# Kernel optimization log

Hardware: AMD Instinct MI355X
Metric: run time of the kernel (lower is better)

Reference implementation:

```python
import jax, jax.numpy as jnp
import numpy as np

N_USER = 50000
N_ITEM = 50000
D_IN = 128
D_OUT = 128
N_EDGE = 600000


def _sage(x_src, x_dst, ei, Wl, bl, Wr):
    # PyG SAGEConv: out = lin_l(mean_{j in N(i)} x_j) + lin_r(x_i)
    # lin_l has bias, lin_r has no bias. Weights are [out, in].
    src, dst = ei[0], ei[1]
    n_dst = x_dst.shape[0]
    msg = x_src[src]                                            # [E, D_in] gather
    agg = jax.ops.segment_sum(msg, dst, num_segments=n_dst)     # [N_dst, D_in]
    cnt = jax.ops.segment_sum(jnp.ones((ei.shape[1],), x_src.dtype), dst,
                              num_segments=n_dst)
    mean = agg / jnp.maximum(cnt, 1.0)[:, None]                 # isolated nodes -> 0
    return mean @ Wl.T + bl + x_dst @ Wr.T


def setup_inputs() -> dict:
    key = jax.random.key(0)
    ks = jax.random.split(key, 16)
    inp = {
        "x_user": jax.random.normal(ks[0], (N_USER, D_IN), jnp.float32),
        "x_item": jax.random.normal(ks[1], (N_ITEM, D_IN), jnp.float32),
        "ei_rates": jax.random.randint(ks[2], (2, N_EDGE), 0, N_USER, jnp.int64 if jax.config.jax_enable_x64 else jnp.int32),
        "ei_rev": jax.random.randint(ks[3], (2, N_EDGE), 0, N_USER, jnp.int64 if jax.config.jax_enable_x64 else jnp.int32),
        "ei_follows": jax.random.randint(ks[4], (2, N_EDGE), 0, N_USER, jnp.int64 if jax.config.jax_enable_x64 else jnp.int32),
    }
    s = 1.0 / np.sqrt(D_IN)
    names = ["rates", "rev", "fol"]
    for i, nm in enumerate(names):
        inp[f"Wl_{nm}"] = jax.random.uniform(ks[5 + 3 * i], (D_OUT, D_IN), jnp.float32, -s, s)
        inp[f"bl_{nm}"] = jax.random.uniform(ks[6 + 3 * i], (D_OUT,), jnp.float32, -s, s)
        inp[f"Wr_{nm}"] = jax.random.uniform(ks[7 + 3 * i], (D_OUT, D_IN), jnp.float32, -s, s)
    return inp


def reference(x_user, x_item, ei_rates, ei_rev, ei_follows,
              Wl_rates, bl_rates, Wr_rates,
              Wl_rev, bl_rev, Wr_rev,
              Wl_fol, bl_fol, Wr_fol):
    # relation (user -rates-> item): src=user, dst=item
    out_item = _sage(x_user, x_item, ei_rates, Wl_rates, bl_rates, Wr_rates)
    # relation (item -rev_rates-> user): src=item, dst=user
    out_user_rev = _sage(x_item, x_user, ei_rev, Wl_rev, bl_rev, Wr_rev)
    # relation (user -follows-> user)
    out_user_fol = _sage(x_user, x_user, ei_follows, Wl_fol, bl_fol, Wr_fol)
    # HeteroConv aggr='mean': average relation outputs per dst node type
    out_user = (out_user_rev + out_user_fol) * 0.5
    return out_user, out_item
```

## Files before the change

kernel.cpp:

```cpp
#include <hip/hip_runtime.h>

#define D 128
#define NBB 392

typedef __attribute__((ext_vector_type(8))) short bf16x8;
typedef __attribute__((ext_vector_type(4))) float f32x4;

__device__ inline unsigned short f2bf(float f) {
  unsigned u = __builtin_bit_cast(unsigned, f);
  unsigned r = u + 0x7FFFu + ((u >> 16) & 1u);
  return (unsigned short)(r >> 16);
}
__device__ inline float bf2f(unsigned short b) {
  unsigned u = ((unsigned)b) << 16;
  return __builtin_bit_cast(float, u);
}

__global__ void __launch_bounds__(256) conv2_kernel(
    const float* __restrict__ xu, const float* __restrict__ xi,
    unsigned short* __restrict__ xbu, unsigned short* __restrict__ xbi,
    int n4u, int n4i) {
  int i = blockIdx.x * 256 + threadIdx.x;
  const float* x;
  unsigned short* xb;
  if (i < n4u) { x = xu; xb = xbu; }
  else { i -= n4u; if (i >= n4i) return; x = xi; xb = xbi; }
  float4 v = ((const float4*)x)[i];
  ushort4 o;
  o.x = f2bf(v.x); o.y = f2bf(v.y); o.z = f2bf(v.z); o.w = f2bf(v.w);
  ((ushort4*)xb)[i] = o;
}

struct Rel3 { const int* ei[3]; int ne[3]; int nb[3]; };

__global__ void __launch_bounds__(256) bhist_kernel(Rel3 R, int* __restrict__ bh) {
  int b = blockIdx.x, rel = 0;
  while (b >= R.nb[rel]) { b -= R.nb[rel]; rel++; }
  __shared__ int lh[NBB];
  for (int t = threadIdx.x; t < NBB; t += 256) lh[t] = 0;
  __syncthreads();
  const int ne = R.ne[rel];
  const int* dsts = R.ei[rel] + ne;
  const int base = b * 2048;
#pragma unroll
  for (int k = 0; k < 8; k++) {
    int i = base + k * 256 + threadIdx.x;
    if (i < ne) atomicAdd(&lh[dsts[i] >> 7], 1);
  }
  __syncthreads();
  for (int t = threadIdx.x; t < NBB; t += 256)
    if (lh[t]) atomicAdd(&bh[rel * NBB + t], lh[t]);
}

__global__ void __launch_bounds__(192) scanb_kernel(const int* __restrict__ bh,
                                                    int* __restrict__ bbase,
                                                    int* __restrict__ bcur, int nbkt) {
  int w = threadIdx.x >> 6, l = threadIdx.x & 63;
  if (w >= 3) return;
  const int off = w * NBB;
  int v[7];
  int s0 = 0;
#pragma unroll
  for (int k = 0; k < 7; k++) {
    int idx = l * 7 + k;
    v[k] = (idx < nbkt) ? bh[off + idx] : 0;
    s0 += v[k];
  }
  int s = s0;
  for (int dlt = 1; dlt < 64; dlt <<= 1) {
    int t = __shfl_up(s, dlt);
    if (l >= dlt) s += t;
  }
  int run = s - s0;
#pragma unroll
  for (int k = 0; k < 7; k++) {
    int idx = l * 7 + k;
    if (idx < nbkt) { bbase[off + idx] = run; bcur[off + idx] = run; run += v[k]; }
  }
  if (l == 63) bbase[off + nbkt] = run;
}

struct PArgs { const int* ei[3]; int ne[3]; int nb[3]; unsigned* part[3]; };

__global__ void __launch_bounds__(256) part_kernel(PArgs P, int* __restrict__ bcur,
                                                   int nbkt) {
  int b = blockIdx.x, rel = 0;
  while (b >= P.nb[rel]) { b -= P.nb[rel]; rel++; }
  const int ne = P.ne[rel];
  const int* src = P.ei[rel];
  const int* dst = src + ne;
  const int base = b * 4096;
  const int tn = min(4096, ne - base);
  __shared__ int lh[NBB], lscan[NBB], gb[NBB], lcur[NBB];
  __shared__ uint2 pairs[4096];
  const int tid = threadIdx.x;
  for (int t = tid; t < NBB; t += 256) lh[t] = 0;
  __syncthreads();
#pragma unroll
  for (int k = 0; k < 16; k++) {
    int i = base + k * 256 + tid;
    if (i < ne) atomicAdd(&lh[dst[i] >> 7], 1);
  }
  __syncthreads();
  if (tid < 64) {
    int v[7];
    int s0 = 0;
#pragma unroll
    for (int k = 0; k < 7; k++) {
      int idx = tid * 7 + k;
      v[k] = (idx < NBB) ? lh[idx] : 0;
      s0 += v[k];
    }
    int s = s0;
    for (int dlt = 1; dlt < 64; dlt <<= 1) {
      int t = __shfl_up(s, dlt);
      if (tid >= dlt) s += t;
    }
    int run = s - s0;
#pragma unroll
    for (int k = 0; k < 7; k++) {
      int idx = tid * 7 + k;
      if (idx < NBB) { lscan[idx] = run; run += v[k]; }
    }
  }
  __syncthreads();
  for (int t = tid; t < nbkt; t += 256) {
    gb[t] = atomicAdd(&bcur[rel * NBB + t], lh[t]);
    lcur[t] = lscan[t];
  }
  __syncthreads();
#pragma unroll
  for (int k = 0; k < 16; k++) {
    int i = base + k * 256 + tid;
    if (i < ne) {
      int d = dst[i];
      int slot = atomicAdd(&lcur[d >> 7], 1);
      pairs[slot] = (uint2){(unsigned)src[i], (unsigned)d};
    }
  }
  __syncthreads();
  unsigned* __restrict__ out = P.part[rel];
#pragma unroll
  for (int k = 0; k < 16; k++) {
    int slot = k * 256 + tid;
    if (slot < tn) {
      uint2 p = pairs[slot];
      int bin = (int)(p.y >> 7);
      out[gb[bin] + (slot - lscan[bin])] = p.x | ((p.y & 127u) << 25);
    }
  }
}

struct S2Args {
  const unsigned* part[3];
  int* rp[3];
  int* es[3];
  int m[3];
};

__global__ void __launch_bounds__(256) sort2_kernel(S2Args A, const int* __restrict__ bbase,
                                                    int nbkt) {
  const int rel = blockIdx.x / nbkt;
  const int b = blockIdx.x - rel * nbkt;
  const int bs = bbase[rel * NBB + b];
  const int be = bbase[rel * NBB + b + 1];
  const int n = be - bs;
  const unsigned* __restrict__ pp = A.part[rel] + bs;
  int* __restrict__ es = A.es[rel];
  const int tid = threadIdx.x;
  __shared__ unsigned stage[4096];
  __shared__ int lcnt[128], lofs[128], lcur[128];
  if (tid < 128) lcnt[tid] = 0;
  __syncthreads();
  const bool staged = (n <= 4096);
  if (staged) {
    for (int i = tid; i < n; i += 256) {
      unsigned p = pp[i];
      stage[i] = p;
      atomicAdd(&lcnt[p >> 25], 1);
    }
  } else {
    for (int i = tid; i < n; i += 256) atomicAdd(&lcnt[pp[i] >> 25], 1);
  }
  __syncthreads();
  if (tid < 64) {
    int v0 = lcnt[2 * tid], v1 = lcnt[2 * tid + 1];
    int s0 = v0 + v1;
    int s = s0;
    for (int dlt = 1; dlt < 64; dlt <<= 1) {
      int t = __shfl_up(s, dlt);
      if (tid >= dlt) s += t;
    }
    int ex = s - s0;
    lofs[2 * tid] = ex;
    lofs[2 * tid + 1] = ex + v0;
  }
  __syncthreads();
  if (tid < 128) {
    int gdst = b * 128 + tid;
    if (gdst < A.m[rel]) A.rp[rel][gdst] = bs + lofs[tid];
    lcur[tid] = lofs[tid];
  }
  if (b == nbkt - 1 && tid == 0) A.rp[rel][A.m[rel]] = bbase[rel * NBB + nbkt];
  __syncthreads();
  if (staged) {
    for (int i = tid; i < n; i += 256) {
      unsigned p = stage[i];
      int slot = atomicAdd(&lcur[p >> 25], 1);
      es[bs + slot] = (int)(p & 0x1FFFFFFu);
    }
  } else {
    for (int i = tid; i < n; i += 256) {
      unsigned p = pp[i];
      int slot = atomicAdd(&lcur[p >> 25], 1);
      es[bs + slot] = (int)(p & 0x1FFFFFFu);
    }
  }
}

struct GatherArgs {
  const unsigned short* xb[3];
  const int* rp[3];
  const int* es[3];
  unsigned short* mean[3];
  int m[3];
  int nb[3];
};

__global__ void __launch_bounds__(256) gather3_kernel(GatherArgs G) {
  int b = blockIdx.x, rel = 0;
  while (b >= G.nb[rel]) { b -= G.nb[rel]; rel++; }
  int row = b * 4 + (threadIdx.x >> 6);
  if (row >= G.m[rel]) return;
  const int lane = threadIdx.x & 63;
  const unsigned short* __restrict__ xb = G.xb[rel];
  const int* __restrict__ rowptr = G.rp[rel];
  const int* __restrict__ esrc = G.es[rel];
  const int beg = rowptr[row], end = rowptr[row + 1];
  const size_t loff = lane * 2;
  float a0 = 0.f, a1 = 0.f, b0 = 0.f, b1 = 0.f;
  float c0 = 0.f, c1 = 0.f, d0 = 0.f, d1 = 0.f;
  int j = beg;
  for (; j + 4 <= end; j += 4) {
    int s0 = esrc[j], s1 = esrc[j + 1], s2 = esrc[j + 2], s3 = esrc[j + 3];
    unsigned v0 = *(const unsigned*)(xb + (size_t)s0 * D + loff);
    unsigned v1 = *(const unsigned*)(xb + (size_t)s1 * D + loff);
    unsigned v2 = *(const unsigned*)(xb + (size_t)s2 * D + loff);
    unsigned v3 = *(const unsigned*)(xb + (size_t)s3 * D + loff);
    a0 += bf2f((unsigned short)(v0 & 0xFFFFu)); a1 += bf2f((unsigned short)(v0 >> 16));
    b0 += bf2f((unsigned short)(v1 & 0xFFFFu)); b1 += bf2f((unsigned short)(v1 >> 16));
    c0 += bf2f((unsigned short)(v2 & 0xFFFFu)); c1 += bf2f((unsigned short)(v2 >> 16));
    d0 += bf2f((unsigned short)(v3 & 0xFFFFu)); d1 += bf2f((unsigned short)(v3 >> 16));
  }
  for (; j < end; j++) {
    int s = esrc[j];
    unsigned v = *(const unsigned*)(xb + (size_t)s * D + loff);
    a0 += bf2f((unsigned short)(v & 0xFFFFu)); a1 += bf2f((unsigned short)(v >> 16));
  }
  a0 += (b0 + c0) + d0;
  a1 += (b1 + c1) + d1;
  float inv = 1.0f / (float)max(end - beg, 1);
  unsigned o = (unsigned)f2bf(a0 * inv) | ((unsigned)f2bf(a1 * inv) << 16);
  *(unsigned*)(G.mean[rel] + (size_t)row * D + loff) = o;
}

__global__ void __launch_bounds__(384) prep_kernel(
    const float* __restrict__ Wl_rates, const float* __restrict__ Wr_rates, const float* __restrict__ bl_rates,
    const float* __restrict__ Wl_rev, const float* __restrict__ Wr_rev, const float* __restrict__ bl_rev,
    const float* __restrict__ Wl_fol, const float* __restrict__ Wr_fol, const float* __restrict__ bl_fol,
    unsigned short* __restrict__ Wb_user, unsigned short* __restrict__ Wb_item,
    float* __restrict__ b_user, float* __restrict__ b_item) {
  int n = blockIdx.x;
  int k = threadIdx.x;
  float v;
  if (k < 128)      v = 0.5f * Wl_rev[n * 128 + k];
  else if (k < 256) v = 0.5f * Wl_fol[n * 128 + (k - 128)];
  else              v = 0.5f * (Wr_rev[n * 128 + (k - 256)] + Wr_fol[n * 128 + (k - 256)]);
  Wb_user[n * 384 + k] = f2bf(v);
  if (k < 256) {
    float w = (k < 128) ? Wl_rates[n * 128 + k] : Wr_rates[n * 128 + (k - 128)];
    Wb_item[n * 256 + k] = f2bf(w);
  }
  if (n == 0 && k < 128) {
    b_item[k] = bl_rates[k];
    b_user[k] = 0.5f * (bl_rev[k] + bl_fol[k]);
  }
}

struct BSrcs { const unsigned short* s[3]; };
struct GemmArgs {
  BSrcs su, si;
  const unsigned short* wbU; const unsigned short* wbI;
  const float* bU; const float* bI;
  float* outU; float* outI;
  int MU, MI, nbU;
};

__global__ void __launch_bounds__(256) gemm2_kernel(GemmArgs A) {
  const bool isU = (int)blockIdx.x < A.nbU;
  const int bid = isU ? blockIdx.x : blockIdx.x - A.nbU;
  const BSrcs S = isU ? A.su : A.si;
  const unsigned short* __restrict__ Wb = isU ? A.wbU : A.wbI;
  const int K = isU ? 384 : 256;
  const float* __restrict__ bias = isU ? A.bU : A.bI;
  float* __restrict__ out = isU ? A.outU : A.outI;
  const int M = isU ? A.MU : A.MI;

  __shared__ __align__(16) unsigned short As[64][72];
  __shared__ __align__(16) unsigned short Ws[128][72];
  const int tid = threadIdx.x;
  const int lane = tid & 63;
  const int wave = tid >> 6;
  const int wrow = (wave >> 1) * 32;
  const int wcol = (wave & 1) * 64;
  const int l15 = lane & 15;
  const int quad = lane >> 4;
  const int m0 = bid * 64;

  f32x4 acc[2][4];
#pragma unroll
  for (int r = 0; r < 2; r++)
#pragma unroll
    for (int c = 0; c < 4; c++) acc[r][c] = (f32x4){0.f, 0.f, 0.f, 0.f};

  const int nchunks = K >> 6;
  for (int ch = 0; ch < nchunks; ch++) {
    const unsigned short* sp = S.s[ch >> 1];
    const int coff = (ch & 1) << 6;
    {
      int row = tid >> 2, part = tid & 3;
      int m = m0 + row;
      uint4 v0 = {0, 0, 0, 0}, v1 = {0, 0, 0, 0};
      if (m < M) {
        const uint4* g = (const uint4*)(sp + (size_t)m * D + coff + part * 16);
        v0 = g[0]; v1 = g[1];
      }
      uint4* ld = (uint4*)(&As[row][part * 16]);
      ld[0] = v0; ld[1] = v1;
    }
    {
      int n = tid >> 1, half = tid & 1;
      const uint4* g = (const uint4*)(Wb + (size_t)n * K + ch * 64 + half * 32);
      uint4* ld = (uint4*)(&Ws[n][half * 32]);
      ld[0] = g[0]; ld[1] = g[1]; ld[2] = g[2]; ld[3] = g[3];
    }
    __syncthreads();
#pragma unroll
    for (int kk = 0; kk < 64; kk += 32) {
      const int kb = kk + quad * 8;
      bf16x8 a0 = *(const bf16x8*)&As[wrow + l15][kb];
      bf16x8 a1 = *(const bf16x8*)&As[wrow + 16 + l15][kb];
      bf16x8 b0 = *(const bf16x8*)&Ws[wcol + l15][kb];
      bf16x8 b1 = *(const bf16x8*)&Ws[wcol + 16 + l15][kb];
      bf16x8 b2 = *(const bf16x8*)&Ws[wcol + 32 + l15][kb];
      bf16x8 b3 = *(const bf16x8*)&Ws[wcol + 48 + l15][kb];
      acc[0][0] = __builtin_amdgcn_mfma_f32_16x16x32_bf16(a0, b0, acc[0][0], 0, 0, 0);
      acc[0][1] = __builtin_amdgcn_mfma_f32_16x16x32_bf16(a0, b1, acc[0][1], 0, 0, 0);
      acc[0][2] = __builtin_amdgcn_mfma_f32_16x16x32_bf16(a0, b2, acc[0][2], 0, 0, 0);
      acc[0][3] = __builtin_amdgcn_mfma_f32_16x16x32_bf16(a0, b3, acc[0][3], 0, 0, 0);
      acc[1][0] = __builtin_amdgcn_mfma_f32_16x16x32_bf16(a1, b0, acc[1][0], 0, 0, 0);
      acc[1][1] = __builtin_amdgcn_mfma_f32_16x16x32_bf16(a1, b1, acc[1][1], 0, 0, 0);
      acc[1][2] = __builtin_amdgcn_mfma_f32_16x16x32_bf16(a1, b2, acc[1][2], 0, 0, 0);
      acc[1][3] = __builtin_amdgcn_mfma_f32_16x16x32_bf16(a1, b3, acc[1][3], 0, 0, 0);
    }
    __syncthreads();
  }
#pragma unroll
  for (int c = 0; c < 4; c++) {
    const int n = wcol + c * 16 + l15;
    const float bv = bias[n];
#pragma unroll
    for (int r = 0; r < 2; r++) {
      const int mrow = m0 + wrow + r * 16 + quad * 4;
#pragma unroll
      for (int i = 0; i < 4; i++) {
        if (mrow + i < M) out[(size_t)(mrow + i) * D + n] = acc[r][c][i] + bv;
      }
    }
  }
}

extern "C" void kernel_launch(void* const* d_in, const int* in_sizes, int n_in,
                              void* d_out, int out_size, void* d_ws, size_t ws_size,
                              hipStream_t stream) {
  const float* x_user   = (const float*)d_in[0];
  const float* x_item   = (const float*)d_in[1];
  const int*   ei_rates = (const int*)d_in[2];
  const int*   ei_rev   = (const int*)d_in[3];
  const int*   ei_fol   = (const int*)d_in[4];
  const float* Wl_rates = (const float*)d_in[5];
  const float* bl_rates = (const float*)d_in[6];
  const float* Wr_rates = (const float*)d_in[7];
  const float* Wl_rev   = (const float*)d_in[8];
  const float* bl_rev   = (const float*)d_in[9];
  const float* Wr_rev   = (const float*)d_in[10];
  const float* Wl_fol   = (const float*)d_in[11];
  const float* bl_fol   = (const float*)d_in[12];
  const float* Wr_fol   = (const float*)d_in[13];

  const int NU = in_sizes[0] / D;
  const int NI = in_sizes[1] / D;
  const int E_rates = in_sizes[2] / 2;
  const int E_rev   = in_sizes[3] / 2;
  const int E_fol   = in_sizes[4] / 2;
  const int nbkt = ((NU > NI ? NU : NI) + 127) / 128;

  char* wsb = (char*)d_ws;
  size_t off = 0;
  auto take = [&](size_t bytes) {
    char* p = wsb + off;
    off += (bytes + 15) & ~(size_t)15;
    return p;
  };
  int* bhist = (int*)take(3 * NBB * 4);
  const size_t zero_bytes = off;
  int* bbase = (int*)take(3 * NBB * 4);
  int* bcur  = (int*)take(3 * NBB * 4);
  unsigned* part_rates = (unsigned*)take((size_t)E_rates * 4);
  unsigned* part_rev   = (unsigned*)take((size_t)E_rev * 4);
  unsigned* part_fol   = (unsigned*)take((size_t)E_fol * 4);
  int* es_rates = (int*)take((size_t)E_rates * 4);
  int* es_rev   = (int*)take((size_t)E_rev * 4);
  int* es_fol   = (int*)take((size_t)E_fol * 4);
  int* rp_rates = (int*)take((size_t)(NI + 1) * 4);
  int* rp_rev   = (int*)take((size_t)(NU + 1) * 4);
  int* rp_fol   = (int*)take((size_t)(NU + 1) * 4);
  unsigned short* xb_user    = (unsigned short*)take((size_t)NU * D * 2);
  unsigned short* xb_item    = (unsigned short*)take((size_t)NI * D * 2);
  unsigned short* mean_rates = (unsigned short*)take((size_t)NI * D * 2);
  unsigned short* mean_rev   = (unsigned short*)take((size_t)NU * D * 2);
  unsigned short* mean_fol   = (unsigned short*)take((size_t)NU * D * 2);
  unsigned short* Wb_user    = (unsigned short*)take(128 * 384 * 2);
  unsigned short* Wb_item    = (unsigned short*)take(128 * 256 * 2);
  float* b_user = (float*)take(128 * 4);
  float* b_item = (float*)take(128 * 4);

  hipMemsetAsync(d_ws, 0, zero_bytes, stream);
  prep_kernel<<<128, 384, 0, stream>>>(Wl_rates, Wr_rates, bl_rates,
                                       Wl_rev, Wr_rev, bl_rev,
                                       Wl_fol, Wr_fol, bl_fol,
                                       Wb_user, Wb_item, b_user, b_item);
  {
    int n4u = NU * D / 4, n4i = NI * D / 4;
    conv2_kernel<<<(n4u + n4i + 255) / 256, 256, 0, stream>>>(
        x_user, x_item, xb_user, xb_item, n4u, n4i);
  }

  Rel3 R;
  R.ei[0] = ei_rates; R.ne[0] = E_rates; R.nb[0] = (E_rates + 2047) / 2048;
  R.ei[1] = ei_rev;   R.ne[1] = E_rev;   R.nb[1] = (E_rev + 2047) / 2048;
  R.ei[2] = ei_fol;   R.ne[2] = E_fol;   R.nb[2] = (E_fol + 2047) / 2048;
  bhist_kernel<<<R.nb[0] + R.nb[1] + R.nb[2], 256, 0, stream>>>(R, bhist);

  scanb_kernel<<<1, 192, 0, stream>>>(bhist, bbase, bcur, nbkt);

  PArgs P;
  P.ei[0] = ei_rates; P.ne[0] = E_rates; P.nb[0] = (E_rates + 4095) / 4096; P.part[0] = part_rates;
  P.ei[1] = ei_rev;   P.ne[1] = E_rev;   P.nb[1] = (E_rev + 4095) / 4096;   P.part[1] = part_rev;
  P.ei[2] = ei_fol;   P.ne[2] = E_fol;   P.nb[2] = (E_fol + 4095) / 4096;   P.part[2] = part_fol;
  part_kernel<<<P.nb[0] + P.nb[1] + P.nb[2], 256, 0, stream>>>(P, bcur, nbkt);

  S2Args S2;
  S2.part[0] = part_rates; S2.rp[0] = rp_rates; S2.es[0] = es_rates; S2.m[0] = NI;
  S2.part[1] = part_rev;   S2.rp[1] = rp_rev;   S2.es[1] = es_rev;   S2.m[1] = NU;
  S2.part[2] = part_fol;   S2.rp[2] = rp_fol;   S2.es[2] = es_fol;   S2.m[2] = NU;
  sort2_kernel<<<3 * nbkt, 256, 0, stream>>>(S2, bbase, nbkt);

  GatherArgs ga;
  ga.xb[0] = xb_user; ga.rp[0] = rp_rates; ga.es[0] = es_rates; ga.mean[0] = mean_rates;
  ga.m[0] = NI; ga.nb[0] = (NI + 3) / 4;
  ga.xb[1] = xb_item; ga.rp[1] = rp_rev;   ga.es[1] = es_rev;   ga.mean[1] = mean_rev;
  ga.m[1] = NU; ga.nb[1] = (NU + 3) / 4;
  ga.xb[2] = xb_user; ga.rp[2] = rp_fol;   ga.es[2] = es_fol;   ga.mean[2] = mean_fol;
  ga.m[2] = NU; ga.nb[2] = (NU + 3) / 4;
  gather3_kernel<<<ga.nb[0] + ga.nb[1] + ga.nb[2], 256, 0, stream>>>(ga);

  GemmArgs gma;
  gma.su.s[0] = mean_rev;   gma.su.s[1] = mean_fol; gma.su.s[2] = xb_user;
  gma.si.s[0] = mean_rates; gma.si.s[1] = xb_item;  gma.si.s[2] = nullptr;
  gma.wbU = Wb_user; gma.wbI = Wb_item;
  gma.bU = b_user;   gma.bI = b_item;
  gma.outU = (float*)d_out;
  gma.outI = (float*)d_out + (size_t)NU * D;
  gma.MU = NU; gma.MI = NI;
  gma.nbU = (NU + 63) / 64;
  const int nbI = (NI + 63) / 64;
  gemm2_kernel<<<gma.nbU + nbI, 256, 0, stream>>>(gma);
}
```

Measured before the change: 313.7 us.

## Fuse bucket sort with neighbor gather and enlarge GEMM row tile

Merges the per-bucket counting sort and the mean-aggregation gather into one kernel. Each block sorts its 128-destination bucket into shared memory and immediately aggregates neighbor features, so the es/rowptr arrays are never written to or read back from global memory and one launch disappears. Each block now handles 128 rows with only 4 waves, which may lower parallelism in the gather phase. Oversized buckets fall back to a slow per-row linear scan. The GEMM tile also doubles to 128 rows per block with 4x4 MFMA accumulators per wave, clamping row loads instead of zero-filling them.

```diff
diff --git a/kernel.cpp b/kernel.cpp
--- a/kernel.cpp
+++ b/kernel.cpp
@@ -151,117 +151,104 @@
   }
 }
 
-struct S2Args {
+struct BAArgs {
   const unsigned* part[3];
-  int* rp[3];
-  int* es[3];
+  const unsigned short* xb[3];
+  unsigned short* mean[3];
   int m[3];
 };
 
-__global__ void __launch_bounds__(256) sort2_kernel(S2Args A, const int* __restrict__ bbase,
-                                                    int nbkt) {
+__global__ void __launch_bounds__(256) bagg_kernel(BAArgs A, const int* __restrict__ bbase,
+                                                   int nbkt) {
   const int rel = blockIdx.x / nbkt;
   const int b = blockIdx.x - rel * nbkt;
   const int bs = bbase[rel * NBB + b];
   const int be = bbase[rel * NBB + b + 1];
   const int n = be - bs;
   const unsigned* __restrict__ pp = A.part[rel] + bs;
-  int* __restrict__ es = A.es[rel];
+  const unsigned short* __restrict__ x = A.xb[rel];
+  unsigned short* __restrict__ mean = A.mean[rel];
+  const int m = A.m[rel];
   const int tid = threadIdx.x;
-  __shared__ unsigned stage[4096];
+  const int w = tid >> 6, lane = tid & 63;
+  const size_t loff = lane * 2;
+  __shared__ unsigned sorted[4096];
   __shared__ int lcnt[128], lofs[128], lcur[128];
-  if (tid < 128) lcnt[tid] = 0;
-  __syncthreads();
-  const bool staged = (n <= 4096);
-  if (staged) {
-    for (int i = tid; i < n; i += 256) {
-      unsigned p = pp[i];
-      stage[i] = p;
-      atomicAdd(&lcnt[p >> 25], 1);
-    }
-  } else {
+
+  if (n <= 4096) {
+    if (tid < 128) lcnt[tid] = 0;
+    __syncthreads();
     for (int i = tid; i < n; i += 256) atomicAdd(&lcnt[pp[i] >> 25], 1);
-  }
-  __syncthreads();
-  if (tid < 64) {
-    int v0 = lcnt[2 * tid], v1 = lcnt[2 * tid + 1];
-    int s0 = v0 + v1;
-    int s = s0;
-    for (int dlt = 1; dlt < 64; dlt <<= 1) {
-      int t = __shfl_up(s, dlt);
-      if (tid >= dlt) s += t;
-    }
-    int ex = s - s0;
-    lofs[2 * tid] = ex;
-    lofs[2 * tid + 1] = ex + v0;
-  }
-  __syncthreads();
-  if (tid < 128) {
-    int gdst = b * 128 + tid;
-    if (gdst < A.m[rel]) A.rp[rel][gdst] = bs + lofs[tid];
-    lcur[tid] = lofs[tid];
-  }
-  if (b == nbkt - 1 && tid == 0) A.rp[rel][A.m[rel]] = bbase[rel * NBB + nbkt];
-  __syncthreads();
-  if (staged) {
-    for (int i = tid; i < n; i += 256) {
-      unsigned p = stage[i];
-      int slot = atomicAdd(&lcur[p >> 25], 1);
-      es[bs + slot] = (int)(p & 0x1FFFFFFu);
-    }
-  } else {
+    __syncthreads();
+    if (tid < 64) {
+      int v0 = lcnt[2 * tid], v1 = lcnt[2 * tid + 1];
+      int s0 = v0 + v1, s = s0;
+      for (int dlt = 1; dlt < 64; dlt <<= 1) {
+        int t = __shfl_up(s, dlt);
+        if (tid >= dlt) s += t;
+      }
+      int ex = s - s0;
+      lofs[2 * tid] = ex;
+      lofs[2 * tid + 1] = ex + v0;
+    }
+    __syncthreads();
+    if (tid < 128) lcur[tid] = lofs[tid];
+    __syncthreads();
     for (int i = tid; i < n; i += 256) {
       unsigned p = pp[i];
       int slot = atomicAdd(&lcur[p >> 25], 1);
-      es[bs + slot] = (int)(p & 0x1FFFFFFu);
-    }
-  }
-}
-
-struct GatherArgs {
-  const unsigned short* xb[3];
-  const int* rp[3];
-  const int* es[3];
-  unsigned short* mean[3];
-  int m[3];
-  int nb[3];
-};
-
-__global__ void __launch_bounds__(256) gather3_kernel(GatherArgs G) {
-  int b = blockIdx.x, rel = 0;
-  while (b >= G.nb[rel]) { b -= G.nb[rel]; rel++; }
-  int row = b * 4 + (threadIdx.x >> 6);
-  if (row >= G.m[rel]) return;
-  const int lane = threadIdx.x & 63;
-  const unsigned short* __restrict__ xb = G.xb[rel];
-  const int* __restrict__ rowptr = G.rp[rel];
-  const int* __restrict__ esrc = G.es[rel];
-  const int beg = rowptr[row], end = rowptr[row + 1];
-  const size_t loff = lane * 2;
-  float a0 = 0.f, a1 = 0.f, b0 = 0.f, b1 = 0.f;
-  float c0 = 0.f, c1 = 0.f, d0 = 0.f, d1 = 0.f;
-  int j = beg;
-  for (; j + 4 <= end; j += 4) {
-    int s0 = esrc[j], s1 = esrc[j + 1], s2 = esrc[j + 2], s3 = esrc[j + 3];
-    unsigned v0 = *(const unsigned*)(xb + (size_t)s0 * D + loff);
-    unsigned v1 = *(const unsigned*)(xb + (size_t)s1 * D + loff);
-    unsigned v2 = *(const unsigned*)(xb + (size_t)s2 * D + loff);
-    unsigned v3 = *(const unsigned*)(xb + (size_t)s3 * D + loff);
-    a0 += bf2f((unsigned short)(v0 & 0xFFFFu)); a1 += bf2f((unsigned short)(v0 >> 16));
-    b0 += bf2f((unsigned short)(v1 & 0xFFFFu)); b1 += bf2f((unsigned short)(v1 >> 16));
-    c0 += bf2f((unsigned short)(v2 & 0xFFFFu)); c1 += bf2f((unsigned short)(v2 >> 16));
-    d0 += bf2f((unsigned short)(v3 & 0xFFFFu)); d1 += bf2f((unsigned short)(v3 >> 16));
-  }
-  for (; j < end; j++) {
-    int s = esrc[j];
-    unsigned v = *(const unsigned*)(xb + (size_t)s * D + loff);
-    a0 += bf2f((unsigned short)(v & 0xFFFFu)); a1 += bf2f((unsigned short)(v >> 16));
-  }
-  a0 += (b0 + c0) + d0;
-  a1 += (b1 + c1) + d1;
-  float inv = 1.0f / (float)max(end - beg, 1);
-  unsigned o = (unsigned)f2bf(a0 * inv) | ((unsigned)f2bf(a1 * inv) << 16);
-  *(unsigned*)(G.mean[rel] + (size_t)row * D + loff) = o;
+      sorted[slot] = p & 0x1FFFFFFu;
+    }
+    __syncthreads();
+    for (int r = w; r < 128; r += 4) {
+      int gdst = b * 128 + r;
+      if (gdst >= m) break;
+      const int beg = lofs[r], end = lcur[r];
+      float a0 = 0.f, a1 = 0.f, b0 = 0.f, b1 = 0.f;
+      float c0 = 0.f, c1 = 0.f, d0 = 0.f, d1 = 0.f;
+      int j = beg;
+      for (; j + 4 <= end; j += 4) {
+        unsigned s0 = sorted[j], s1 = sorted[j + 1], s2 = sorted[j + 2], s3 = sorted[j + 3];
+        unsigned v0 = *(const unsigned*)(x + (size_t)s0 * D + loff);
+        unsigned v1 = *(const unsigned*)(x + (size_t)s1 * D + loff);
+        unsigned v2 = *(const unsigned*)(x + (size_t)s2 * D + loff);
+        unsigned v3 = *(const unsigned*)(x + (size_t)s3 * D + loff);
+        a0 += bf2f((unsigned short)(v0 & 0xFFFFu)); a1 += bf2f((unsigned short)(v0 >> 16));
+        b0 += bf2f((unsigned short)(v1 & 0xFFFFu)); b1 += bf2f((unsigned short)(v1 >> 16));
+        c0 += bf2f((unsigned short)(v2 & 0xFFFFu)); c1 += bf2f((unsigned short)(v2 >> 16));
+        d0 += bf2f((unsigned short)(v3 & 0xFFFFu)); d1 += bf2f((unsigned short)(v3 >> 16));
+      }
+      for (; j < end; j++) {
+        unsigned s = sorted[j];
+        unsigned v = *(const unsigned*)(x + (size_t)s * D + loff);
+        a0 += bf2f((unsigned short)(v & 0xFFFFu)); a1 += bf2f((unsigned short)(v >> 16));
+      }
+      a0 += (b0 + c0) + d0;
+      a1 += (b1 + c1) + d1;
+      float inv = 1.0f / (float)max(end - beg, 1);
+      unsigned o = (unsigned)f2bf(a0 * inv) | ((unsigned)f2bf(a1 * inv) << 16);
+      *(unsigned*)(mean + (size_t)gdst * D + loff) = o;
+    }
+  } else {
+    for (int r = w; r < 128; r += 4) {
+      int gdst = b * 128 + r;
+      if (gdst >= m) break;
+      float a0 = 0.f, a1 = 0.f;
+      int cnt = 0;
+      for (int j = 0; j < n; j++) {
+        unsigned p = pp[j];
+        if ((int)(p >> 25) == r) {
+          unsigned v = *(const unsigned*)(x + (size_t)(p & 0x1FFFFFFu) * D + loff);
+          a0 += bf2f((unsigned short)(v & 0xFFFFu));
+          a1 += bf2f((unsigned short)(v >> 16));
+          cnt++;
+        }
+      }
+      float inv = 1.0f / (float)max(cnt, 1);
+      unsigned o = (unsigned)f2bf(a0 * inv) | ((unsigned)f2bf(a1 * inv) << 16);
+      *(unsigned*)(mean + (size_t)gdst * D + loff) = o;
+    }
+  }
 }
 
 __global__ void __launch_bounds__(384) prep_kernel(
@@ -306,54 +293,51 @@
   float* __restrict__ out = isU ? A.outU : A.outI;
   const int M = isU ? A.MU : A.MI;
 
-  __shared__ __align__(16) unsigned short As[64][72];
+  __shared__ __align__(16) unsigned short As[128][72];
   __shared__ __align__(16) unsigned short Ws[128][72];
   const int tid = threadIdx.x;
   const int lane = tid & 63;
   const int wave = tid >> 6;
-  const int wrow = (wave >> 1) * 32;
-  const int wcol = (wave & 1) * 64;
+  const int wr = (wave >> 1) * 64;
+  const int wc = (wave & 1) * 64;
   const int l15 = lane & 15;
   const int quad = lane >> 4;
-  const int m0 = bid * 64;
-
-  f32x4 acc[2][4];
-#pragma unroll
-  for (int r = 0; r < 2; r++)
+  const int m0 = bid * 128;
+
+  f32x4 acc[4][4];
+#pragma unroll
+  for (int r = 0; r < 4; r++)
 #pragma unroll
     for (int c = 0; c < 4; c++) acc[r][c] = (f32x4){0.f, 0.f, 0.f, 0.f};
 
+  const int srow = tid >> 1, shalf = tid & 1;
   const int nchunks = K >> 6;
   for (int ch = 0; ch < nchunks; ch++) {
     const unsigned short* sp = S.s[ch >> 1];
     const int coff = (ch & 1) << 6;
     {
-      int row = tid >> 2, part = tid & 3;
-      int m = m0 + row;
-      uint4 v0 = {0, 0, 0, 0}, v1 = {0, 0, 0, 0};
-      if (m < M) {
-        const uint4* g = (const uint4*)(sp + (size_t)m * D + coff + part * 16);
-        v0 = g[0]; v1 = g[1];
-      }
-      uint4* ld = (uint4*)(&As[row][part * 16]);
-      ld[0] = v0; ld[1] = v1;
+      int mm = min(m0 + srow, M - 1);
+      const uint4* g = (const uint4*)(sp + (size_t)mm * D + coff + shalf * 32);
+      uint4* ld = (uint4*)(&As[srow][shalf * 32]);
+      ld[0] = g[0]; ld[1] = g[1]; ld[2] = g[2]; ld[3] = g[3];
     }
     {
-      int n = tid >> 1, half = tid & 1;
-      const uint4* g = (const uint4*)(Wb + (size_t)n * K + ch * 64 + half * 32);
-      uint4* ld = (uint4*)(&Ws[n][half * 32]);
+      const uint4* g = (const uint4*)(Wb + (size_t)srow * K + ch * 64 + shalf * 32);
+      uint4* ld = (uint4*)(&Ws[srow][shalf * 32]);
       ld[0] = g[0]; ld[1] = g[1]; ld[2] = g[2]; ld[3] = g[3];
     }
     __syncthreads();
 #pragma unroll
     for (int kk = 0; kk < 64; kk += 32) {
       const int kb = kk + quad * 8;
-      bf16x8 a0 = *(const bf16x8*)&As[wrow + l15][kb];
-      bf16x8 a1 = *(const bf16x8*)&As[wrow + 16 + l15][kb];
-      bf16x8 b0 = *(const bf16x8*)&Ws[wcol + l15][kb];
-      bf16x8 b1 = *(const bf16x8*)&Ws[wcol + 16 + l15][kb];
-      bf16x8 b2 = *(const bf16x8*)&Ws[wcol + 32 + l15][kb];
-      bf16x8 b3 = *(const bf16x8*)&Ws[wcol + 48 + l15][kb];
+      bf16x8 a0 = *(const bf16x8*)&As[wr + l15][kb];
+      bf16x8 a1 = *(const bf16x8*)&As[wr + 16 + l15][kb];
+      bf16x8 a2 = *(const bf16x8*)&As[wr + 32 + l15][kb];
+      bf16x8 a3 = *(const bf16x8*)&As[wr + 48 + l15][kb];
+      bf16x8 b0 = *(const bf16x8*)&Ws[wc + l15][kb];
+      bf16x8 b1 = *(const bf16x8*)&Ws[wc + 16 + l15][kb];
+      bf16x8 b2 = *(const bf16x8*)&Ws[wc + 32 + l15][kb];
+      bf16x8 b3 = *(const bf16x8*)&Ws[wc + 48 + l15][kb];
       acc[0][0] = __builtin_amdgcn_mfma_f32_16x16x32_bf16(a0, b0, acc[0][0], 0, 0, 0);
       acc[0][1] = __builtin_amdgcn_mfma_f32_16x16x32_bf16(a0, b1, acc[0][1], 0, 0, 0);
       acc[0][2] = __builtin_amdgcn_mfma_f32_16x16x32_bf16(a0, b2, acc[0][2], 0, 0, 0);
@@ -362,16 +346,24 @@
       acc[1][1] = __builtin_amdgcn_mfma_f32_16x16x32_bf16(a1, b1, acc[1][1], 0, 0, 0);
       acc[1][2] = __builtin_amdgcn_mfma_f32_16x16x32_bf16(a1, b2, acc[1][2], 0, 0, 0);
       acc[1][3] = __builtin_amdgcn_mfma_f32_16x16x32_bf16(a1, b3, acc[1][3], 0, 0, 0);
+      acc[2][0] = __builtin_amdgcn_mfma_f32_16x16x32_bf16(a2, b0, acc[2][0], 0, 0, 0);
+      acc[2][1] = __builtin_amdgcn_mfma_f32_16x16x32_bf16(a2, b1, acc[2][1], 0, 0, 0);
+      acc[2][2] = __builtin_amdgcn_mfma_f32_16x16x32_bf16(a2, b2, acc[2][2], 0, 0, 0);
+      acc[2][3] = __builtin_amdgcn_mfma_f32_16x16x32_bf16(a2, b3, acc[2][3], 0, 0, 0);
+      acc[3][0] = __builtin_amdgcn_mfma_f32_16x16x32_bf16(a3, b0, acc[3][0], 0, 0, 0);
+      acc[3][1] = __builtin_amdgcn_mfma_f32_16x16x32_bf16(a3, b1, acc[3][1], 0, 0, 0);
+      acc[3][2] = __builtin_amdgcn_mfma_f32_16x16x32_bf16(a3, b2, acc[3][2], 0, 0, 0);
+      acc[3][3] = __builtin_amdgcn_mfma_f32_16x16x32_bf16(a3, b3, acc[3][3], 0, 0, 0);
     }
     __syncthreads();
   }
 #pragma unroll
   for (int c = 0; c < 4; c++) {
-    const int n = wcol + c * 16 + l15;
+    const int n = wc + c * 16 + l15;
     const float bv = bias[n];
 #pragma unroll
-    for (int r = 0; r < 2; r++) {
-      const int mrow = m0 + wrow + r * 16 + quad * 4;
+    for (int r = 0; r < 4; r++) {
+      const int mrow = m0 + wr + r * 16 + quad * 4;
 #pragma unroll
       for (int i = 0; i < 4; i++) {
         if (mrow + i < M) out[(size_t)(mrow + i) * D + n] = acc[r][c][i] + bv;
@@ -419,12 +411,6 @@
   unsigned* part_rates = (unsigned*)take((size_t)E_rates * 4);
   unsigned* part_rev   = (unsigned*)take((size_t)E_rev * 4);
   unsigned* part_fol   = (unsigned*)take((size_t)E_fol * 4);
-  int* es_rates = (int*)take((size_t)E_rates * 4);
-  int* es_rev   = (int*)take((size_t)E_rev * 4);
-  int* es_fol   = (int*)take((size_t)E_fol * 4);
-  int* rp_rates = (int*)take((size_t)(NI + 1) * 4);
-  int* rp_rev   = (int*)take((size_t)(NU + 1) * 4);
-  int* rp_fol   = (int*)take((size_t)(NU + 1) * 4);
   unsigned short* xb_user    = (unsigned short*)take((size_t)NU * D * 2);
   unsigned short* xb_item    = (unsigned short*)take((size_t)NI * D * 2);
   unsigned short* mean_rates = (unsigned short*)take((size_t)NI * D * 2);
@@ -460,20 +446,11 @@
   P.ei[2] = ei_fol;   P.ne[2] = E_fol;   P.nb[2] = (E_fol + 4095) / 4096;   P.part[2] = part_fol;
   part_kernel<<<P.nb[0] + P.nb[1] + P.nb[2], 256, 0, stream>>>(P, bcur, nbkt);
 
-  S2Args S2;
-  S2.part[0] = part_rates; S2.rp[0] = rp_rates; S2.es[0] = es_rates; S2.m[0] = NI;
-  S2.part[1] = part_rev;   S2.rp[1] = rp_rev;   S2.es[1] = es_rev;   S2.m[1] = NU;
-  S2.part[2] = part_fol;   S2.rp[2] = rp_fol;   S2.es[2] = es_fol;   S2.m[2] = NU;
-  sort2_kernel<<<3 * nbkt, 256, 0, stream>>>(S2, bbase, nbkt);
-
-  GatherArgs ga;
-  ga.xb[0] = xb_user; ga.rp[0] = rp_rates; ga.es[0] = es_rates; ga.mean[0] = mean_rates;
-  ga.m[0] = NI; ga.nb[0] = (NI + 3) / 4;
-  ga.xb[1] = xb_item; ga.rp[1] = rp_rev;   ga.es[1] = es_rev;   ga.mean[1] = mean_rev;
-  ga.m[1] = NU; ga.nb[1] = (NU + 3) / 4;
-  ga.xb[2] = xb_user; ga.rp[2] = rp_fol;   ga.es[2] = es_fol;   ga.mean[2] = mean_fol;
-  ga.m[2] = NU; ga.nb[2] = (NU + 3) / 4;
-  gather3_kernel<<<ga.nb[0] + ga.nb[1] + ga.nb[2], 256, 0, stream>>>(ga);
+  BAArgs BA;
+  BA.part[0] = part_rates; BA.xb[0] = xb_user; BA.mean[0] = mean_rates; BA.m[0] = NI;
+  BA.part[1] = part_rev;   BA.xb[1] = xb_item; BA.mean[1] = mean_rev;   BA.m[1] = NU;
+  BA.part[2] = part_fol;   BA.xb[2] = xb_user; BA.mean[2] = mean_fol;   BA.m[2] = NU;
+  bagg_kernel<<<3 * nbkt, 256, 0, stream>>>(BA, bbase, nbkt);
 
   GemmArgs gma;
   gma.su.s[0] = mean_rev;   gma.su.s[1] = mean_fol; gma.su.s[2] = xb_user;
@@ -483,7 +460,7 @@
   gma.outU = (float*)d_out;
   gma.outI = (float*)d_out + (size_t)NU * D;
   gma.MU = NU; gma.MI = NI;
-  gma.nbU = (NU + 63) / 64;
-  const int nbI = (NI + 63) / 64;
+  gma.nbU = (NU + 127) / 128;
+  const int nbI = (NI + 127) / 128;
   gemm2_kernel<<<gma.nbU + nbI, 256, 0, stream>>>(gma);
 }
```

Result: no change. 314.0 us (+0.1%).
